# Performance work log

Hardware: AMD Instinct MI355X
Metric: run time of the kernel (lower is better)

The kernel has to match this reference:

```python
import jax, jax.numpy as jnp
import numpy as np

EPS = 1e-8
ANGULAR_WEIGHT = 0.1
L2_REG = 1e-4


def gram_schmidt_batch(A):
    # A: (B, 3, 3); orthogonalize the COLUMNS
    u1 = A[:, :, 0]
    e1 = u1 / (jnp.linalg.norm(u1, axis=1, keepdims=True) + EPS)
    a2 = A[:, :, 1]
    u2 = a2 - jnp.sum(e1 * a2, axis=1, keepdims=True) * e1
    e2 = u2 / (jnp.linalg.norm(u2, axis=1, keepdims=True) + EPS)
    a3 = A[:, :, 2]
    u3 = a3 - jnp.sum(e1 * a3, axis=1, keepdims=True) * e1 - jnp.sum(e2 * a3, axis=1, keepdims=True) * e2
    e3 = u3 / (jnp.linalg.norm(u3, axis=1, keepdims=True) + EPS)
    Q = jnp.stack([e1, e2, e3], axis=2)  # (B,3,3), columns e1,e2,e3
    det = jnp.linalg.det(Q)
    # flip third column where det < 0 to ensure proper rotation
    e3_fixed = jnp.where(det[:, None] < 0, -Q[:, :, 2], Q[:, :, 2])
    return Q.at[:, :, 2].set(e3_fixed)


def nine_d_to_rotmat(nine_d):
    A = jnp.clip(nine_d, -10.0, 10.0).reshape(-1, 3, 3)
    return gram_schmidt_batch(A)


def angular_distance(pred_9d, target_9d):
    pred_rot = nine_d_to_rotmat(pred_9d)
    target_rot = nine_d_to_rotmat(target_9d)
    # trace(pred^T @ target) = sum over all entries of elementwise product
    traces = jnp.einsum('bij,bij->b', pred_rot, target_rot)
    traces = jnp.clip(traces, -3.0 + 1e-6, 3.0 - 1e-6)
    cos_angle = jnp.clip((traces - 1.0) / 2.0, -1.0 + 1e-7, 1.0 - 1e-7)
    angles_deg = jnp.arccos(cos_angle) * (180.0 / np.pi)
    return jnp.where(jnp.isnan(angles_deg), 180.0, angles_deg)


def orthogonality_loss(nine_d):
    B = nine_d.shape[0]
    M = nine_d.reshape(B, 3, 3)
    AtA = jnp.einsum('bki,bkj->bij', M, M)
    diff = AtA - jnp.eye(3, dtype=nine_d.dtype)
    return jnp.mean(jnp.sum(diff * diff, axis=(1, 2)))


def setup_inputs() -> dict:
    key = jax.random.key(0)
    k1, k2 = jax.random.split(key)
    B = 4194304
    return {
        'pred_delta_9d': jax.random.normal(k1, (B, 9), dtype=jnp.float32),
        'target_delta_9d': jax.random.normal(k2, (B, 9), dtype=jnp.float32),
    }


def reference(pred_delta_9d, target_delta_9d):
    pred_delta_9d = jnp.clip(pred_delta_9d, -10.0, 10.0)
    pred_rot = nine_d_to_rotmat(pred_delta_9d)
    target_rot = nine_d_to_rotmat(target_delta_9d)
    diff = pred_rot - target_rot
    chordal_loss = jnp.mean(jnp.sum(diff * diff, axis=(1, 2)))
    angular_loss_term = jnp.mean(angular_distance(pred_delta_9d, target_delta_9d))
    ortho_loss = orthogonality_loss(pred_delta_9d)
    l2_loss = jnp.mean(pred_delta_9d ** 2)
    total_loss = chordal_loss + ANGULAR_WEIGHT * angular_loss_term + 0.01 * ortho_loss + L2_REG * l2_loss
    # NaN fallback: MSE between pred and target
    fallback = jnp.mean((pred_delta_9d - target_delta_9d) ** 2)
    return jnp.where(jnp.isnan(total_loss), fallback, total_loss)
```

## Files before the change

### kernel.cpp

```cpp
#include <hip/hip_runtime.h>
#include <math.h>

#define EPS_GS 1e-8f
#define RAD2DEG 57.29577951308232f
#define PI_F 3.14159265358979f

constexpr int THREADS   = 256;
constexpr int TILE_ROTS = 512;
constexpr int TILE_F    = TILE_ROTS * 9;
constexpr int TILE_F2   = TILE_F / 2;
constexpr int F2_PER_TH = TILE_F2 / THREADS;
constexpr int NSLOTS    = 16;

__device__ __forceinline__ float clip10(float x) {
    x = x < -10.f ? -10.f : x;
    x = x >  10.f ?  10.f : x;
    return x;
}

__device__ __forceinline__ float fsqrt(float x) { return __builtin_amdgcn_sqrtf(x); }
__device__ __forceinline__ float frcp(float x)  { return __builtin_amdgcn_rcpf(x); }

__device__ __forceinline__ float fast_acos(float x) {
    float ax = fabsf(x);
    float p = fmaf(ax, -0.0187293f, 0.0742610f);
    p = fmaf(ax, p, -0.2121144f);
    p = fmaf(ax, p, 1.5707288f);
    float pos = fsqrt(1.f - ax) * p;
    return x >= 0.f ? pos : PI_F - pos;
}

__device__ __forceinline__ void gs_rotmat(const float* v, float* R) {
    float c0x = v[0], c0y = v[3], c0z = v[6];
    float c1x = v[1], c1y = v[4], c1z = v[7];
    float c2x = v[2], c2y = v[5], c2z = v[8];

    float s1 = fmaf(c0x, c0x, fmaf(c0y, c0y, c0z*c0z));
    float inv1 = frcp(fsqrt(s1) + EPS_GS);
    float e1x = c0x*inv1, e1y = c0y*inv1, e1z = c0z*inv1;

    float d = fmaf(e1x, c1x, fmaf(e1y, c1y, e1z*c1z));
    float u2x = fmaf(-d, e1x, c1x), u2y = fmaf(-d, e1y, c1y), u2z = fmaf(-d, e1z, c1z);
    float s2 = fmaf(u2x, u2x, fmaf(u2y, u2y, u2z*u2z));
    float inv2 = frcp(fsqrt(s2) + EPS_GS);
    float e2x = u2x*inv2, e2y = u2y*inv2, e2z = u2z*inv2;

    float d1 = fmaf(e1x, c2x, fmaf(e1y, c2y, e1z*c2z));
    float d2 = fmaf(e2x, c2x, fmaf(e2y, c2y, e2z*c2z));
    float u3x = fmaf(-d1, e1x, fmaf(-d2, e2x, c2x));
    float u3y = fmaf(-d1, e1y, fmaf(-d2, e2y, c2y));
    float u3z = fmaf(-d1, e1z, fmaf(-d2, e2z, c2z));
    float s3 = fmaf(u3x, u3x, fmaf(u3y, u3y, u3z*u3z));
    float inv3 = frcp(fsqrt(s3) + EPS_GS);
    float e3x = u3x*inv3, e3y = u3y*inv3, e3z = u3z*inv3;

    float cxx = e2y*e3z - e2z*e3y;
    float cxy = e2z*e3x - e2x*e3z;
    float cxz = e2x*e3y - e2y*e3x;
    float det = fmaf(e1x, cxx, fmaf(e1y, cxy, e1z*cxz));
    if (det < 0.f) { e3x = -e3x; e3y = -e3y; e3z = -e3z; }

    R[0] = e1x; R[1] = e2x; R[2] = e3x;
    R[3] = e1y; R[4] = e2y; R[5] = e3y;
    R[6] = e1z; R[7] = e2z; R[8] = e3z;
}

__device__ __forceinline__ void accum_rot(const float* pr, const float* tg,
                                          float& lt, float& lf) {
    float pc[9], tc[9];
    #pragma unroll
    for (int m = 0; m < 9; ++m) { pc[m] = clip10(pr[m]); tc[m] = clip10(tg[m]); }

    float Rp[9], Rt[9];
    gs_rotmat(pc, Rp);
    gs_rotmat(tc, Rt);

    float chord = 0.f, tr = 0.f;
    #pragma unroll
    for (int m = 0; m < 9; ++m) {
        float d = Rp[m] - Rt[m];
        chord = fmaf(d, d, chord);
        tr    = fmaf(Rp[m], Rt[m], tr);
    }

    const float trLo = -3.0f + 1e-6f, trHi = 3.0f - 1e-6f;
    tr = tr < trLo ? trLo : (tr > trHi ? trHi : tr);
    float ca = (tr - 1.f) * 0.5f;
    const float cLo = -1.0f + 1e-7f, cHi = 1.0f - 1e-7f;
    ca = ca < cLo ? cLo : (ca > cHi ? cHi : ca);
    float ang = fast_acos(ca) * RAD2DEG;
    if (ang != ang) ang = 180.f;

    float o = 0.f;
    #pragma unroll
    for (int i = 0; i < 3; ++i) {
        float dii = fmaf(pc[i], pc[i], fmaf(pc[3+i], pc[3+i], pc[6+i]*pc[6+i])) - 1.f;
        o = fmaf(dii, dii, o);
    }
    #pragma unroll
    for (int i = 0; i < 3; ++i) {
        #pragma unroll
        for (int j = i + 1; j < 3; ++j) {
            float s = fmaf(pc[i], pc[j], fmaf(pc[3+i], pc[3+j], pc[6+i]*pc[6+j]));
            float s2 = s + s;
            o = fmaf(s2, s, o);
        }
    }

    float l2 = 0.f, fb = 0.f;
    #pragma unroll
    for (int m = 0; m < 9; ++m) {
        l2 = fmaf(pc[m], pc[m], l2);
        float d = pc[m] - tg[m];
        fb = fmaf(d, d, fb);
    }

    lt += fmaf(0.1f, ang, chord) + fmaf(0.01f, o, (1e-4f/9.f)*l2);
    lf += fb;
}

__global__ __launch_bounds__(THREADS, 4)
void rot_loss_kernel(const float* __restrict__ pred, const float* __restrict__ targ,
                     double* __restrict__ acc, int B) {
    __shared__ float sp[TILE_F];
    __shared__ float sq[TILE_F];
    __shared__ float rsum_t[4], rsum_f[4];

    const int tid = threadIdx.x;
    const long long rot0 = (long long)blockIdx.x * TILE_ROTS;
    const long long rem64 = (long long)B - rot0;
    const int rem = rem64 > TILE_ROTS ? TILE_ROTS : (int)rem64;

    float lt = 0.f, lf = 0.f;

    if (rem == TILE_ROTS) {
        const float2* p2 = reinterpret_cast<const float2*>(pred + rot0 * 9);
        const float2* q2 = reinterpret_cast<const float2*>(targ + rot0 * 9);
        float2 pv[F2_PER_TH], tv[F2_PER_TH];
        #pragma unroll
        for (int k = 0; k < F2_PER_TH; ++k) pv[k] = p2[tid + k*THREADS];
        #pragma unroll
        for (int k = 0; k < F2_PER_TH; ++k) tv[k] = q2[tid + k*THREADS];
        float2* sp2 = reinterpret_cast<float2*>(sp);
        float2* sq2 = reinterpret_cast<float2*>(sq);
        #pragma unroll
        for (int k = 0; k < F2_PER_TH; ++k) {
            sp2[tid + k*THREADS] = pv[k];
            sq2[tid + k*THREADS] = tv[k];
        }
        __syncthreads();
        #pragma unroll
        for (int rr = 0; rr < 2; ++rr) {
            const int r = tid + rr*THREADS;
            accum_rot(&sp[9*r], &sq[9*r], lt, lf);
        }
    } else if (rem > 0) {
        for (int r = tid; r < rem; r += THREADS) {
            float a1[9], b1[9];
            const float* pp = pred + (rot0 + r) * 9;
            const float* qq = targ + (rot0 + r) * 9;
            for (int m = 0; m < 9; ++m) { a1[m] = pp[m]; b1[m] = qq[m]; }
            accum_rot(a1, b1, lt, lf);
        }
    }

    #pragma unroll
    for (int off = 32; off > 0; off >>= 1) {
        lt += __shfl_down(lt, off, 64);
        lf += __shfl_down(lf, off, 64);
    }
    const int lane = tid & 63;
    const int wid  = tid >> 6;
    if (lane == 0) { rsum_t[wid] = lt; rsum_f[wid] = lf; }
    __syncthreads();
    if (tid == 0) {
        float bt = rsum_t[0] + rsum_t[1] + rsum_t[2] + rsum_t[3];
        float bf = rsum_f[0] + rsum_f[1] + rsum_f[2] + rsum_f[3];
        double* slot = acc + (size_t)(blockIdx.x & (NSLOTS - 1)) * 8;
        unsafeAtomicAdd(&slot[0], (double)bt);
        unsafeAtomicAdd(&slot[1], (double)bf);
    }
}

__global__ void finalize_kernel(const double* __restrict__ acc,
                                float* __restrict__ out, int B) {
    if (threadIdx.x == 0 && blockIdx.x == 0) {
        double t = 0.0, f = 0.0;
        for (int s = 0; s < NSLOTS; ++s) { t += acc[s*8]; f += acc[s*8 + 1]; }
        double total = t / (double)B;
        double fb    = f / (9.0 * (double)B);
        out[0] = isnan(total) ? (float)fb : (float)total;
    }
}

extern "C" void kernel_launch(void* const* d_in, const int* in_sizes, int n_in,
                              void* d_out, int out_size, void* d_ws, size_t ws_size,
                              hipStream_t stream) {
    const float* pred = (const float*)d_in[0];
    const float* targ = (const float*)d_in[1];
    const int n = in_sizes[0];
    const int B = n / 9;

    double* acc = (double*)d_ws;
    hipMemsetAsync(d_ws, 0, NSLOTS * 8 * sizeof(double), stream);

    const int blocks = (B + TILE_ROTS - 1) / TILE_ROTS;
    rot_loss_kernel<<<blocks, THREADS, 0, stream>>>(pred, targ, acc, B);
    finalize_kernel<<<1, 64, 0, stream>>>(acc, (float*)d_out, B);
}
```

Baseline: 309.4 us.

## Use persistent grid-stride blocks with register prefetch of the next tile

Caps the grid at 1024 blocks and has each block loop over tiles, issuing global loads for the next tile into registers while it computes the current tile from LDS. The aim is to overlap memory latency with the Gram-Schmidt math and to cut block launch and atomic overhead. In exchange, fewer resident waves are available to hide latency, and each tile now needs an extra barrier.

```diff
diff --git a/kernel.cpp b/kernel.cpp
--- a/kernel.cpp
+++ b/kernel.cpp
@@ -11,6 +11,7 @@
 constexpr int TILE_F2   = TILE_F / 2;
 constexpr int F2_PER_TH = TILE_F2 / THREADS;
 constexpr int NSLOTS    = 16;
+constexpr int MAX_BLKS  = 1024;
 
 __device__ __forceinline__ float clip10(float x) {
     x = x < -10.f ? -10.f : x;
@@ -126,41 +127,56 @@
     __shared__ float sq[TILE_F];
     __shared__ float rsum_t[4], rsum_f[4];
 
-    const int tid = threadIdx.x;
-    const long long rot0 = (long long)blockIdx.x * TILE_ROTS;
-    const long long rem64 = (long long)B - rot0;
-    const int rem = rem64 > TILE_ROTS ? TILE_ROTS : (int)rem64;
+    const int tid    = threadIdx.x;
+    const int ntiles = (B + TILE_ROTS - 1) / TILE_ROTS;
 
     float lt = 0.f, lf = 0.f;
 
-    if (rem == TILE_ROTS) {
-        const float2* p2 = reinterpret_cast<const float2*>(pred + rot0 * 9);
-        const float2* q2 = reinterpret_cast<const float2*>(targ + rot0 * 9);
-        float2 pv[F2_PER_TH], tv[F2_PER_TH];
+    float2 pv[F2_PER_TH], tv[F2_PER_TH];
+
+    auto issue_loads = [&](int t) {
+        const float2* p2 = reinterpret_cast<const float2*>(pred) + (size_t)t * TILE_F2;
+        const float2* q2 = reinterpret_cast<const float2*>(targ) + (size_t)t * TILE_F2;
         #pragma unroll
         for (int k = 0; k < F2_PER_TH; ++k) pv[k] = p2[tid + k*THREADS];
         #pragma unroll
         for (int k = 0; k < F2_PER_TH; ++k) tv[k] = q2[tid + k*THREADS];
-        float2* sp2 = reinterpret_cast<float2*>(sp);
-        float2* sq2 = reinterpret_cast<float2*>(sq);
-        #pragma unroll
-        for (int k = 0; k < F2_PER_TH; ++k) {
-            sp2[tid + k*THREADS] = pv[k];
-            sq2[tid + k*THREADS] = tv[k];
-        }
-        __syncthreads();
-        #pragma unroll
-        for (int rr = 0; rr < 2; ++rr) {
-            const int r = tid + rr*THREADS;
-            accum_rot(&sp[9*r], &sq[9*r], lt, lf);
-        }
-    } else if (rem > 0) {
-        for (int r = tid; r < rem; r += THREADS) {
-            float a1[9], b1[9];
-            const float* pp = pred + (rot0 + r) * 9;
-            const float* qq = targ + (rot0 + r) * 9;
-            for (int m = 0; m < 9; ++m) { a1[m] = pp[m]; b1[m] = qq[m]; }
-            accum_rot(a1, b1, lt, lf);
+    };
+    auto tile_full = [&](int t) {
+        return (size_t)(t + 1) * TILE_ROTS <= (size_t)B;
+    };
+
+    int t0 = blockIdx.x;
+    if (t0 < ntiles && tile_full(t0)) issue_loads(t0);
+
+    for (int t = t0; t < ntiles; t += gridDim.x) {
+        const size_t rot0 = (size_t)t * TILE_ROTS;
+        if (tile_full(t)) {
+            float2* sp2 = reinterpret_cast<float2*>(sp);
+            float2* sq2 = reinterpret_cast<float2*>(sq);
+            #pragma unroll
+            for (int k = 0; k < F2_PER_TH; ++k) {
+                sp2[tid + k*THREADS] = pv[k];
+                sq2[tid + k*THREADS] = tv[k];
+            }
+            __syncthreads();
+            const int tn = t + gridDim.x;
+            if (tn < ntiles && tile_full(tn)) issue_loads(tn);
+            #pragma unroll
+            for (int rr = 0; rr < 2; ++rr) {
+                const int r = tid + rr*THREADS;
+                accum_rot(&sp[9*r], &sq[9*r], lt, lf);
+            }
+            __syncthreads();
+        } else {
+            const int rem = (int)((size_t)B - rot0);
+            for (int r = tid; r < rem; r += THREADS) {
+                float a1[9], b1[9];
+                const float* pp = pred + (rot0 + r) * 9;
+                const float* qq = targ + (rot0 + r) * 9;
+                for (int m = 0; m < 9; ++m) { a1[m] = pp[m]; b1[m] = qq[m]; }
+                accum_rot(a1, b1, lt, lf);
+            }
         }
     }
 
@@ -204,7 +220,8 @@
     double* acc = (double*)d_ws;
     hipMemsetAsync(d_ws, 0, NSLOTS * 8 * sizeof(double), stream);
 
-    const int blocks = (B + TILE_ROTS - 1) / TILE_ROTS;
+    const int ntiles = (B + TILE_ROTS - 1) / TILE_ROTS;
+    const int blocks = ntiles < MAX_BLKS ? ntiles : MAX_BLKS;
     rot_loss_kernel<<<blocks, THREADS, 0, stream>>>(pred, targ, acc, B);
     finalize_kernel<<<1, 64, 0, stream>>>(acc, (float*)d_out, B);
 }
```

After: 378.9 us. +22.5%, slower.
